# Kernel tuning notes

Measured on AMD Instinct MI355X. Metric: run time of the kernel, lower is better.

The kernel has to match this reference:

```python
import jax, jax.numpy as jnp
import numpy as np

B, N, C = 2, 8192, 768
H, K = 12, 256
D = C // H
HID = 4 * C
EPS = 1e-6

def layer_norm(x, w, b):
    mu = jnp.mean(x, axis=-1, keepdims=True)
    var = jnp.mean(jnp.square(x - mu), axis=-1, keepdims=True)
    return (x - mu) * jax.lax.rsqrt(var + EPS) * w + b

def setup_inputs() -> dict:
    key = jax.random.key(0)
    ks = jax.random.split(key, 8)
    s = 0.02
    return {
        "x": jax.random.normal(ks[0], (B, N, C), jnp.float32),
        "ln1_w": jnp.ones((C,), jnp.float32),
        "ln1_b": jnp.zeros((C,), jnp.float32),
        "qkv_w": jax.random.normal(ks[1], (C, 3 * C), jnp.float32) * s,
        "qkv_b": jnp.zeros((3 * C,), jnp.float32),
        "Ek": jax.random.normal(ks[2], (N, K), jnp.float32) * s,
        "Ev": jax.random.normal(ks[3], (N, K), jnp.float32) * s,
        "proj_w": jax.random.normal(ks[4], (C, C), jnp.float32) * s,
        "proj_b": jnp.zeros((C,), jnp.float32),
        "ln2_w": jnp.ones((C,), jnp.float32),
        "ln2_b": jnp.zeros((C,), jnp.float32),
        "fc1_w": jax.random.normal(ks[5], (C, HID), jnp.float32) * s,
        "fc1_b": jnp.zeros((HID,), jnp.float32),
        "fc2_w": jax.random.normal(ks[6], (HID, C), jnp.float32) * s,
        "fc2_b": jnp.zeros((C,), jnp.float32),
    }

def reference(x, ln1_w, ln1_b, qkv_w, qkv_b, Ek, Ev, proj_w, proj_b,
              ln2_w, ln2_b, fc1_w, fc1_b, fc2_w, fc2_b):
    scale = D ** -0.5
    # --- attention branch ---
    h = layer_norm(x, ln1_w, ln1_b)
    qkv = h @ qkv_w + qkv_b                      # (B,N,3C)
    qkv = qkv.reshape(B, N, 3, H, D).transpose(2, 0, 3, 1, 4)  # (3,B,H,N,D)
    q, k, v = qkv[0], qkv[1], qkv[2]
    # Linformer: project K/V along sequence dim N -> K
    k_proj = jnp.einsum('bhnd,nk->bhkd', k, Ek)
    v_proj = jnp.einsum('bhnd,nk->bhkd', v, Ev)
    logits = jnp.einsum('bhnd,bhkd->bhnk', q, k_proj) * scale
    logits = jnp.clip(logits, -50.0, 50.0)
    attn = jax.nn.softmax(logits, axis=-1)
    o = jnp.einsum('bhnk,bhkd->bhnd', attn, v_proj)
    o = o.transpose(0, 2, 1, 3).reshape(B, N, C)
    o = o @ proj_w + proj_b
    x = x + o                                    # alpha_attn = 1.0
    # --- MLP branch ---
    h = layer_norm(x, ln2_w, ln2_b)
    h = jax.nn.gelu(h @ fc1_w + fc1_b, approximate=False)
    h = h @ fc2_w + fc2_b
    return x + h                                 # alpha_mlp = 1.0
```

## Files before the change

### kernel.cpp

```cpp
#include <hip/hip_runtime.h>
#include <cstdint>

#define DEV __device__ __forceinline__

typedef __bf16 bf16x8 __attribute__((ext_vector_type(8)));
typedef float f32x4 __attribute__((ext_vector_type(4)));

DEV uint16_t f2bf(float f) {
  uint32_t u = __float_as_uint(f);
  u += 0x7FFFu + ((u >> 16) & 1u);
  return (uint16_t)(u >> 16);
}
DEV float bf2f(uint16_t h) { return __uint_as_float(((uint32_t)h) << 16); }

DEV void gload16(const void* g, void* l) {
  __builtin_amdgcn_global_load_lds((const __attribute__((address_space(1))) void*)g,
                                   (__attribute__((address_space(3))) void*)l, 16, 0, 0);
}

template <int N> DEV void waitcnt_vm() {
  if constexpr (N == 0) asm volatile("s_waitcnt vmcnt(0)" ::: "memory");
  else if constexpr (N == 4) asm volatile("s_waitcnt vmcnt(4)" ::: "memory");
  else if constexpr (N == 6) asm volatile("s_waitcnt vmcnt(6)" ::: "memory");
  else static_assert(N == 0 || N == 4 || N == 6, "unsupported vmcnt");
}

DEV float gelu_f(float v) {
  float u = v * (0.7978845608f + 0.0356774081f * v * v);
  return v / (1.f + __expf(-2.f * u));
}

__global__ __launch_bounds__(256) void ln768(const float* __restrict__ x,
                                             const float* __restrict__ w,
                                             const float* __restrict__ b,
                                             uint16_t* __restrict__ out) {
  const size_t row = blockIdx.x;
  const float* xr = x + row * 768;
  const int t = threadIdx.x;
  float v0 = xr[t], v1 = xr[t + 256], v2 = xr[t + 512];
  float s = v0 + v1 + v2;
  float s2 = v0 * v0 + v1 * v1 + v2 * v2;
#pragma unroll
  for (int o = 32; o; o >>= 1) {
    s += __shfl_down(s, o);
    s2 += __shfl_down(s2, o);
  }
  __shared__ float sh[8];
  if ((t & 63) == 0) { sh[t >> 6] = s; sh[4 + (t >> 6)] = s2; }
  __syncthreads();
  s = sh[0] + sh[1] + sh[2] + sh[3];
  s2 = sh[4] + sh[5] + sh[6] + sh[7];
  const float mu = s * (1.f / 768.f);
  const float var = s2 * (1.f / 768.f) - mu * mu;
  const float rstd = rsqrtf(var + 1e-6f);
  uint16_t* orow = out + row * 768;
  orow[t]       = f2bf((v0 - mu) * rstd * w[t] + b[t]);
  orow[t + 256] = f2bf((v1 - mu) * rstd * w[t + 256] + b[t + 256]);
  orow[t + 512] = f2bf((v2 - mu) * rstd * w[t + 512] + b[t + 512]);
}

__global__ __launch_bounds__(256) void transpose_f2b(const float* __restrict__ in,
                                                     uint16_t* __restrict__ outp,
                                                     int ldin, int ldout) {
  __shared__ float tile[32][33];
  const int tx = threadIdx.x, ty = threadIdx.y;
  const size_t x = (size_t)blockIdx.x * 32 + tx;
  const size_t y = (size_t)blockIdx.y * 32 + ty;
#pragma unroll
  for (int j = 0; j < 4; ++j) tile[ty + j * 8][tx] = in[(y + j * 8) * ldin + x];
  __syncthreads();
  const size_t x2 = (size_t)blockIdx.y * 32 + tx;
  const size_t y2 = (size_t)blockIdx.x * 32 + ty;
#pragma unroll
  for (int j = 0; j < 4; ++j) outp[(y2 + j * 8) * ldout + x2] = f2bf(tile[tx][ty + j * 8]);
}

__global__ __launch_bounds__(256) void transpose_b2b(const uint16_t* __restrict__ in,
                                                     uint16_t* __restrict__ outp,
                                                     int ldin, int ldout) {
  __shared__ uint16_t tile[32][33];
  const int tx = threadIdx.x, ty = threadIdx.y;
  const size_t x = (size_t)blockIdx.x * 32 + tx;
  const size_t y = (size_t)blockIdx.y * 32 + ty;
#pragma unroll
  for (int j = 0; j < 4; ++j) tile[ty + j * 8][tx] = in[(y + j * 8) * ldin + x];
  __syncthreads();
  const size_t x2 = (size_t)blockIdx.y * 32 + tx;
  const size_t y2 = (size_t)blockIdx.x * 32 + ty;
#pragma unroll
  for (int j = 0; j < 4; ++j) outp[(y2 + j * 8) * ldout + x2] = tile[tx][ty + j * 8];
}

__global__ __launch_bounds__(256) void kv_tn(const uint16_t* __restrict__ EkT,
                                             const uint16_t* __restrict__ EvT,
                                             const uint16_t* __restrict__ qkv,
                                             float* __restrict__ part) {
  const int bid = blockIdx.x;
  const int wg = (bid & 7) * 96 + (bid >> 3);
  const int inner = wg & 15;
  const int kt = inner & 3, ns = inner >> 2;
  const int rest = wg >> 4;
  const int ct = rest % 12, kvb = rest / 12;
  const int kv = kvb >> 1, b = kvb & 1;
  const int k0 = kt * 64, c0 = ct * 64, nsb = ns * 2048;

  const uint16_t* E = kv ? EvT : EkT;
  const uint16_t* KV = qkv + (size_t)b * 8192 * 2304 + 768 + kv * 768 + c0;
  const int tid = threadIdx.x, wave = tid >> 6, lane = tid & 63;
  const int l16 = lane & 15, lhi = lane >> 4;
  const int wm = wave >> 1, wn = wave & 1;

  f32x4 acc[2][2];
#pragma unroll
  for (int m = 0; m < 2; ++m)
#pragma unroll
    for (int n = 0; n < 2; ++n) acc[m][n] = f32x4{0.f, 0.f, 0.f, 0.f};

  const uint16_t* Eb = E + (size_t)(k0 + wm * 32 + l16) * 8192 + nsb + lhi * 8;
  const uint16_t* KVb = KV + ((size_t)nsb + lhi * 8) * 2304 + wn * 32 + l16;

  for (int n0 = 0; n0 < 2048; n0 += 32) {
    bf16x8 ef[2];
    ef[0] = *(const bf16x8*)(Eb + n0);
    ef[1] = *(const bf16x8*)(Eb + 16 * 8192 + n0);
    bf16x8 vf[2];
#pragma unroll
    for (int nf = 0; nf < 2; ++nf) {
      const uint16_t* p = KVb + (size_t)n0 * 2304 + nf * 16;
      union { bf16x8 v; uint16_t u[8]; } tu;
#pragma unroll
      for (int j = 0; j < 8; ++j) tu.u[j] = p[(size_t)j * 2304];
      vf[nf] = tu.v;
    }
#pragma unroll
    for (int m = 0; m < 2; ++m)
#pragma unroll
      for (int nf = 0; nf < 2; ++nf)
        acc[m][nf] = __builtin_amdgcn_mfma_f32_16x16x32_bf16(ef[m], vf[nf], acc[m][nf], 0, 0, 0);
  }

  float* outp = part + ((size_t)ns * 4 + kvb) * 196608;
#pragma unroll
  for (int m = 0; m < 2; ++m)
#pragma unroll
    for (int nf = 0; nf < 2; ++nf)
#pragma unroll
      for (int r = 0; r < 4; ++r)
        outp[(size_t)(k0 + wm * 32 + m * 16 + lhi * 4 + r) * 768 + c0 + wn * 32 + nf * 16 + l16] =
            acc[m][nf][r];
}

__global__ __launch_bounds__(256) void kv_reduce(const float* __restrict__ part,
                                                 uint16_t* __restrict__ kproj) {
  const int kvb = blockIdx.y;
  const int i = blockIdx.x * 256 + threadIdx.x;
  const float* p = part + (size_t)kvb * 196608 + i;
  float s = p[0] + p[786432] + p[2 * 786432] + p[3 * 786432];
  kproj[(size_t)kvb * 196608 + i] = f2bf(s);
}

__global__ __launch_bounds__(256, 3) void attn_fused(
    const uint16_t* __restrict__ qkv,
    const uint16_t* __restrict__ kproj,
    const uint16_t* __restrict__ vprojT,
    uint16_t* __restrict__ o) {
  const int bh = blockIdx.y;
  const int b = bh / 12, h = bh % 12;
  const int n0 = blockIdx.x * 64;
  const int tid = threadIdx.x, wave = tid >> 6, lane = tid & 63;
  const int l16 = lane & 15, lhi = lane >> 4;
  const int wm = wave >> 1, wn = wave & 1;

  __shared__ __align__(16) uint16_t sP[64 * 256];
  __shared__ float redm[2][64], reds[2][64], recs[64];

  const uint16_t* Kp = kproj + (size_t)b * 196608 + h * 64;
  const uint16_t* Qp = qkv + ((size_t)b * 8192 + n0) * 2304 + h * 64;
  const uint16_t* Vp = vprojT + ((size_t)b * 768 + h * 64) * 256;

  f32x4 st[8][2];
#pragma unroll
  for (int m = 0; m < 8; ++m)
#pragma unroll
    for (int nf = 0; nf < 2; ++nf) st[m][nf] = f32x4{0.f, 0.f, 0.f, 0.f};
#pragma unroll
  for (int ks = 0; ks < 2; ++ks) {
    bf16x8 kf[8], qf[2];
#pragma unroll
    for (int m = 0; m < 8; ++m) {
      const int kvi = wm * 128 + m * 16 + l16;
      kf[m] = *(const bf16x8*)(Kp + (size_t)kvi * 768 + ks * 32 + lhi * 8);
    }
#pragma unroll
    for (int nf = 0; nf < 2; ++nf) {
      const int n = wn * 32 + nf * 16 + l16;
      qf[nf] = *(const bf16x8*)(Qp + (size_t)n * 2304 + ks * 32 + lhi * 8);
    }
#pragma unroll
    for (int m = 0; m < 8; ++m)
#pragma unroll
      for (int nf = 0; nf < 2; ++nf)
        st[m][nf] = __builtin_amdgcn_mfma_f32_16x16x32_bf16(kf[m], qf[nf], st[m][nf], 0, 0, 0);
  }

  float pmax[2] = {-50.f, -50.f};
#pragma unroll
  for (int m = 0; m < 8; ++m)
#pragma unroll
    for (int nf = 0; nf < 2; ++nf)
#pragma unroll
      for (int r = 0; r < 4; ++r) {
        float v = fminf(fmaxf(st[m][nf][r] * 0.125f, -50.f), 50.f);
        st[m][nf][r] = v;
        pmax[nf] = fmaxf(pmax[nf], v);
      }
#pragma unroll
  for (int nf = 0; nf < 2; ++nf) {
    pmax[nf] = fmaxf(pmax[nf], __shfl_xor(pmax[nf], 16));
    pmax[nf] = fmaxf(pmax[nf], __shfl_xor(pmax[nf], 32));
  }
  if (lhi == 0) {
#pragma unroll
    for (int nf = 0; nf < 2; ++nf) redm[wm][wn * 32 + nf * 16 + l16] = pmax[nf];
  }
  __syncthreads();
  float M[2];
#pragma unroll
  for (int nf = 0; nf < 2; ++nf) {
    const int col = wn * 32 + nf * 16 + l16;
    M[nf] = fmaxf(redm[0][col], redm[1][col]);
  }

  float psum[2] = {0.f, 0.f};
#pragma unroll
  for (int m = 0; m < 8; ++m) {
#pragma unroll
    for (int nf = 0; nf < 2; ++nf) {
      float e0 = __expf(st[m][nf][0] - M[nf]);
      float e1 = __expf(st[m][nf][1] - M[nf]);
      float e2 = __expf(st[m][nf][2] - M[nf]);
      float e3 = __expf(st[m][nf][3] - M[nf]);
      psum[nf] += (e0 + e1) + (e2 + e3);
      uint2 pk;
      pk.x = (uint32_t)f2bf(e0) | ((uint32_t)f2bf(e1) << 16);
      pk.y = (uint32_t)f2bf(e2) | ((uint32_t)f2bf(e3) << 16);
      const int n = wn * 32 + nf * 16 + l16;
      const int kvb2 = (wm * 128 + m * 16 + lhi * 4) * 2;
      *(uint2*)((char*)sP + n * 512 + (kvb2 ^ ((n & 7) << 4))) = pk;
    }
  }
#pragma unroll
  for (int nf = 0; nf < 2; ++nf) {
    psum[nf] += __shfl_xor(psum[nf], 16);
    psum[nf] += __shfl_xor(psum[nf], 32);
  }
  if (lhi == 0) {
#pragma unroll
    for (int nf = 0; nf < 2; ++nf) reds[wm][wn * 32 + nf * 16 + l16] = psum[nf];
  }
  __syncthreads();
  if (wm == 0 && lhi == 0) {
#pragma unroll
    for (int nf = 0; nf < 2; ++nf) {
      const int col = wn * 32 + nf * 16 + l16;
      recs[col] = 1.f / (reds[0][col] + reds[1][col]);
    }
  }
  __syncthreads();

  f32x4 pacc[2][2];
#pragma unroll
  for (int mf = 0; mf < 2; ++mf)
#pragma unroll
    for (int nf = 0; nf < 2; ++nf) pacc[mf][nf] = f32x4{0.f, 0.f, 0.f, 0.f};
#pragma unroll
  for (int ks = 0; ks < 8; ++ks) {
    bf16x8 pa[2], vb[2];
#pragma unroll
    for (int mf = 0; mf < 2; ++mf) {
      const int n = wm * 32 + mf * 16 + l16;
      pa[mf] = *(const bf16x8*)((char*)sP + n * 512 + ((ks * 64 + lhi * 16) ^ ((n & 7) << 4)));
    }
#pragma unroll
    for (int nf = 0; nf < 2; ++nf) {
      const int d = wn * 32 + nf * 16 + l16;
      vb[nf] = *(const bf16x8*)(Vp + (size_t)d * 256 + ks * 32 + lhi * 8);
    }
#pragma unroll
    for (int mf = 0; mf < 2; ++mf)
#pragma unroll
      for (int nf = 0; nf < 2; ++nf)
        pacc[mf][nf] = __builtin_amdgcn_mfma_f32_16x16x32_bf16(pa[mf], vb[nf], pacc[mf][nf], 0, 0, 0);
  }
  uint16_t* orow = o + ((size_t)b * 8192 + n0) * 768 + h * 64;
#pragma unroll
  for (int mf = 0; mf < 2; ++mf) {
#pragma unroll
    for (int r = 0; r < 4; ++r) {
      const int n = wm * 32 + mf * 16 + lhi * 4 + r;
      const float inv = recs[n];
#pragma unroll
      for (int nf = 0; nf < 2; ++nf) {
        const int d = wn * 32 + nf * 16 + l16;
        orow[(size_t)n * 768 + d] = f2bf(pacc[mf][nf][r] * inv);
      }
    }
  }
}

template <int BM, int BN, bool OUTBF, bool HASBIAS, bool DOGELU, bool HASRES>
__global__ __launch_bounds__(512, 2) void gemm3(
    const uint16_t* __restrict__ A, const uint16_t* __restrict__ B,
    void* __restrict__ Cbase, const float* __restrict__ bias,
    const float* __restrict__ res, int Kd, int lda, int ldb, int ldc) {
  constexpr int WROWS = BM / 4, WCOLS = BN / 2;
  constexpr int FM = WROWS / 16, FN = WCOLS / 16;
  constexpr int IA = BM / 64, IB = BN / 64;
  constexpr int LPT = IA + IB;
  constexpr int ABUF = BM * 64, BBUF = BN * 64;
  __shared__ __align__(16) uint16_t lds[3 * (ABUF + BBUF)];

  const int nn = gridDim.y;
  const int nwg = gridDim.x * gridDim.y;
  const int bid = blockIdx.y * gridDim.x + blockIdx.x;
  const int q = nwg >> 3, r8 = nwg & 7, xcd = bid & 7, idx = bid >> 3;
  const int wg = (xcd < r8 ? xcd * (q + 1) : r8 * (q + 1) + (xcd - r8) * q) + idx;
  const int bm = wg / nn, bn = wg % nn;
  const int row0 = bm * BM, col0 = bn * BN;

  const int tid = threadIdx.x;
  const int wave = tid >> 6, lane = tid & 63;
  const int wm = wave >> 1, wn = wave & 1;
  const int l16 = lane & 15, lhi = lane >> 4;
  const int srow = tid >> 3, sslot = tid & 7;

  auto stageA = [&](uint16_t* sa, int k0, int j) {
    const int rw = j * 64 + srow;
    const int sp = sslot ^ (rw & 7);
    gload16(A + (size_t)(row0 + rw) * lda + k0 + sp * 8, sa + rw * 64 + sslot * 8);
  };
  auto stageB = [&](uint16_t* sb, int k0, int j) {
    const int rw = j * 64 + srow;
    const int sp = sslot ^ (rw & 7);
    gload16(B + (size_t)(col0 + rw) * ldb + k0 + sp * 8, sb + rw * 64 + sslot * 8);
  };

  f32x4 acc[FM][FN];
#pragma unroll
  for (int m = 0; m < FM; ++m)
#pragma unroll
    for (int n = 0; n < FN; ++n) acc[m][n] = f32x4{0.f, 0.f, 0.f, 0.f};

  const int NT = Kd >> 6;
#pragma unroll
  for (int j = 0; j < IA; ++j) stageA(lds, 0, j);
#pragma unroll
  for (int j = 0; j < IB; ++j) stageB(lds + ABUF, 0, j);
#pragma unroll
  for (int j = 0; j < IA; ++j) stageA(lds + (ABUF + BBUF), 64, j);
#pragma unroll
  for (int j = 0; j < IB; ++j) stageB(lds + (ABUF + BBUF) + ABUF, 64, j);

  for (int t = 0; t < NT; ++t) {
    if (t < NT - 1) waitcnt_vm<LPT>();
    else waitcnt_vm<0>();
    __builtin_amdgcn_s_barrier();
    asm volatile("" ::: "memory");
    const uint16_t* sa = lds + (t % 3) * (ABUF + BBUF);
    const uint16_t* sb = sa + ABUF;
    uint16_t* pa = lds + ((t + 2) % 3) * (ABUF + BBUF);
    uint16_t* pb = pa + ABUF;
    const bool pf = (t + 2) < NT;
    const int k0p = (t + 2) * 64;

    if (pf) {
#pragma unroll
      for (int j = 0; j < IA / 2; ++j) stageA(pa, k0p, j);
#pragma unroll
      for (int j = 0; j < IB / 2; ++j) stageB(pb, k0p, j);
    }
    {
      bf16x8 af[FM], bfr[FN];
#pragma unroll
      for (int n = 0; n < FN; ++n) {
        const int rw = wn * WCOLS + n * 16 + l16;
        bfr[n] = *(const bf16x8*)(sb + rw * 64 + ((lhi) ^ (rw & 7)) * 8);
      }
#pragma unroll
      for (int m = 0; m < FM; ++m) {
        const int rw = wm * WROWS + m * 16 + l16;
        af[m] = *(const bf16x8*)(sa + rw * 64 + ((lhi) ^ (rw & 7)) * 8);
      }
      __builtin_amdgcn_s_setprio(1);
#pragma unroll
      for (int m = 0; m < FM; ++m)
#pragma unroll
        for (int n = 0; n < FN; ++n)
          acc[m][n] = __builtin_amdgcn_mfma_f32_16x16x32_bf16(af[m], bfr[n], acc[m][n], 0, 0, 0);
      __builtin_amdgcn_s_setprio(0);
    }
    if (pf) {
#pragma unroll
      for (int j = IA / 2; j < IA; ++j) stageA(pa, k0p, j);
#pragma unroll
      for (int j = IB / 2; j < IB; ++j) stageB(pb, k0p, j);
    }
    {
      bf16x8 af[FM], bfr[FN];
#pragma unroll
      for (int n = 0; n < FN; ++n) {
        const int rw = wn * WCOLS + n * 16 + l16;
        bfr[n] = *(const bf16x8*)(sb + rw * 64 + ((4 + lhi) ^ (rw & 7)) * 8);
      }
#pragma unroll
      for (int m = 0; m < FM; ++m) {
        const int rw = wm * WROWS + m * 16 + l16;
        af[m] = *(const bf16x8*)(sa + rw * 64 + ((4 + lhi) ^ (rw & 7)) * 8);
      }
      __builtin_amdgcn_s_setprio(1);
#pragma unroll
      for (int m = 0; m < FM; ++m)
#pragma unroll
        for (int n = 0; n < FN; ++n)
          acc[m][n] = __builtin_amdgcn_mfma_f32_16x16x32_bf16(af[m], bfr[n], acc[m][n], 0, 0, 0);
      __builtin_amdgcn_s_setprio(0);
    }
  }

  float* Cf = (float*)Cbase;
  uint16_t* Cb = (uint16_t*)Cbase;
#pragma unroll
  for (int m = 0; m < FM; ++m) {
#pragma unroll
    for (int n = 0; n < FN; ++n) {
      const int col = col0 + wn * WCOLS + n * 16 + l16;
      float bv = 0.f;
      if (HASBIAS) bv = bias[col];
#pragma unroll
      for (int r = 0; r < 4; ++r) {
        const int row = row0 + wm * WROWS + m * 16 + lhi * 4 + r;
        float v = acc[m][n][r] + bv;
        if (DOGELU) v = gelu_f(v);
        const size_t cidx = (size_t)row * ldc + col;
        if (HASRES) v += res[cidx];
        if (OUTBF) Cb[cidx] = f2bf(v);
        else Cf[cidx] = v;
      }
    }
  }
}

extern "C" void kernel_launch(void* const* d_in, const int* in_sizes, int n_in,
                              void* d_out, int out_size, void* d_ws, size_t ws_size,
                              hipStream_t stream) {
  const float* x      = (const float*)d_in[0];
  const float* ln1_w  = (const float*)d_in[1];
  const float* ln1_b  = (const float*)d_in[2];
  const float* qkv_w  = (const float*)d_in[3];
  const float* qkv_b  = (const float*)d_in[4];
  const float* Ek     = (const float*)d_in[5];
  const float* Ev     = (const float*)d_in[6];
  const float* proj_w = (const float*)d_in[7];
  const float* proj_b = (const float*)d_in[8];
  const float* ln2_w  = (const float*)d_in[9];
  const float* ln2_b  = (const float*)d_in[10];
  const float* fc1_w  = (const float*)d_in[11];
  const float* fc1_b  = (const float*)d_in[12];
  const float* fc2_w  = (const float*)d_in[13];
  const float* fc2_b  = (const float*)d_in[14];
  float* out = (float*)d_out;

  char* w8 = (char*)d_ws;
  size_t off = 0;
  auto take = [&](size_t bytes) { char* p = w8 + off; off += bytes; return p; };
  uint16_t* qkv_wT  = (uint16_t*)take(2304ull * 768 * 2);
  uint16_t* proj_wT = (uint16_t*)take(768ull * 768 * 2);
  uint16_t* fc1_wT  = (uint16_t*)take(3072ull * 768 * 2);
  uint16_t* fc2_wT  = (uint16_t*)take(768ull * 3072 * 2);
  uint16_t* EkT     = (uint16_t*)take(256ull * 8192 * 2);
  uint16_t* EvT     = (uint16_t*)take(256ull * 8192 * 2);
  uint16_t* h_bf    = (uint16_t*)take(16384ull * 768 * 2);
  uint16_t* qkv_bf  = (uint16_t*)take(16384ull * 2304 * 2);
  uint16_t* big     = (uint16_t*)take(100663296ull);
  uint16_t* kproj   = (uint16_t*)take(2ull * 2 * 256 * 768 * 2);
  uint16_t* vprojT  = (uint16_t*)take(2ull * 768 * 256 * 2);
  uint16_t* o_bf    = (uint16_t*)take(16384ull * 768 * 2);
  float* part = (float*)big;
  (void)ws_size; (void)in_sizes; (void)n_in; (void)out_size;

  const dim3 tb(32, 8);
  transpose_f2b<<<dim3(72, 24), tb, 0, stream>>>(qkv_w, qkv_wT, 2304, 768);
  transpose_f2b<<<dim3(24, 24), tb, 0, stream>>>(proj_w, proj_wT, 768, 768);
  transpose_f2b<<<dim3(96, 24), tb, 0, stream>>>(fc1_w, fc1_wT, 3072, 768);
  transpose_f2b<<<dim3(24, 96), tb, 0, stream>>>(fc2_w, fc2_wT, 768, 3072);
  transpose_f2b<<<dim3(8, 256), tb, 0, stream>>>(Ek, EkT, 256, 8192);
  transpose_f2b<<<dim3(8, 256), tb, 0, stream>>>(Ev, EvT, 256, 8192);
  ln768<<<16384, 256, 0, stream>>>(x, ln1_w, ln1_b, h_bf);
  gemm3<256, 128, true, true, false, false><<<dim3(64, 18), 512, 0, stream>>>(
      h_bf, qkv_wT, qkv_bf, qkv_b, nullptr, 768, 768, 768, 2304);
  kv_tn<<<768, 256, 0, stream>>>(EkT, EvT, qkv_bf, part);
  kv_reduce<<<dim3(768, 4), 256, 0, stream>>>(part, kproj);
  for (int b = 0; b < 2; ++b)
    transpose_b2b<<<dim3(24, 8), tb, 0, stream>>>(
        kproj + (size_t)(2 + b) * 196608, vprojT + (size_t)b * 768 * 256, 768, 256);
  attn_fused<<<dim3(128, 24), 256, 0, stream>>>(qkv_bf, kproj, vprojT, o_bf);
  gemm3<128, 128, false, true, false, true><<<dim3(128, 6), 512, 0, stream>>>(
      o_bf, proj_wT, out, proj_b, x, 768, 768, 768, 768);
  ln768<<<16384, 256, 0, stream>>>(out, ln2_w, ln2_b, h_bf);
  gemm3<256, 128, true, true, true, false><<<dim3(64, 24), 512, 0, stream>>>(
      h_bf, fc1_wT, big, fc1_b, nullptr, 768, 768, 768, 3072);
  gemm3<128, 128, false, true, false, true><<<dim3(128, 6), 512, 0, stream>>>(
      big, fc2_wT, out, fc2_b, out, 3072, 3072, 3072, 768);
}
```

Measured before the change: 489.9 us.

## Replace GEMM kernels with 256x256-tile double-buffered GEMM using split-K half planes

The templated triple-buffered GEMM is replaced by a fixed 256x256 tile kernel with an 8-wave 2x4 layout. Each 64-wide K tile is staged as two 32-wide half planes into a double buffer with a new swizzle, and loads of the next tile are interleaved with the MFMA sub-steps under more barriers. Larger tiles raise arithmetic intensity and cut global traffic per FLOP. In exchange the grids shrink a lot (e.g. 192 blocks for the proj/fc2 GEMMs on a 256-CU part), which risks underfilling the GPU, and the 128-accumulator register footprint is higher.

```diff
diff --git a/kernel.cpp b/kernel.cpp
--- a/kernel.cpp
+++ b/kernel.cpp
@@ -21,8 +21,7 @@
 template <int N> DEV void waitcnt_vm() {
   if constexpr (N == 0) asm volatile("s_waitcnt vmcnt(0)" ::: "memory");
   else if constexpr (N == 4) asm volatile("s_waitcnt vmcnt(4)" ::: "memory");
-  else if constexpr (N == 6) asm volatile("s_waitcnt vmcnt(6)" ::: "memory");
-  else static_assert(N == 0 || N == 4 || N == 6, "unsupported vmcnt");
+  else static_assert(N == 0 || N == 4, "unsupported vmcnt");
 }
 
 DEV float gelu_f(float v) {
@@ -160,10 +159,8 @@
 }
 
 __global__ __launch_bounds__(256, 3) void attn_fused(
-    const uint16_t* __restrict__ qkv,
-    const uint16_t* __restrict__ kproj,
-    const uint16_t* __restrict__ vprojT,
-    uint16_t* __restrict__ o) {
+    const uint16_t* __restrict__ qkv, const uint16_t* __restrict__ kproj,
+    const uint16_t* __restrict__ vprojT, uint16_t* __restrict__ o) {
   const int bh = blockIdx.y;
   const int b = bh / 12, h = bh % 12;
   const int n0 = blockIdx.x * 64;
@@ -308,17 +305,14 @@
   }
 }
 
-template <int BM, int BN, bool OUTBF, bool HASBIAS, bool DOGELU, bool HASRES>
-__global__ __launch_bounds__(512, 2) void gemm3(
+template <bool OUTBF, bool HASBIAS, bool DOGELU, bool HASRES>
+__global__ __launch_bounds__(512, 2) void gemm256(
     const uint16_t* __restrict__ A, const uint16_t* __restrict__ B,
     void* __restrict__ Cbase, const float* __restrict__ bias,
     const float* __restrict__ res, int Kd, int lda, int ldb, int ldc) {
-  constexpr int WROWS = BM / 4, WCOLS = BN / 2;
-  constexpr int FM = WROWS / 16, FN = WCOLS / 16;
-  constexpr int IA = BM / 64, IB = BN / 64;
-  constexpr int LPT = IA + IB;
-  constexpr int ABUF = BM * 64, BBUF = BN * 64;
-  __shared__ __align__(16) uint16_t lds[3 * (ABUF + BBUF)];
+  constexpr int PLANE = 8192;
+  constexpr int BUF = 4 * PLANE;
+  __shared__ __align__(16) uint16_t lds[2 * BUF];
 
   const int nn = gridDim.y;
   const int nwg = gridDim.x * gridDim.y;
@@ -326,119 +320,98 @@
   const int q = nwg >> 3, r8 = nwg & 7, xcd = bid & 7, idx = bid >> 3;
   const int wg = (xcd < r8 ? xcd * (q + 1) : r8 * (q + 1) + (xcd - r8) * q) + idx;
   const int bm = wg / nn, bn = wg % nn;
-  const int row0 = bm * BM, col0 = bn * BN;
+  const int row0 = bm * 256, col0 = bn * 256;
 
   const int tid = threadIdx.x;
   const int wave = tid >> 6, lane = tid & 63;
-  const int wm = wave >> 1, wn = wave & 1;
+  const int wm = wave >> 2, wn = wave & 3;
   const int l16 = lane & 15, lhi = lane >> 4;
-  const int srow = tid >> 3, sslot = tid & 7;
-
-  auto stageA = [&](uint16_t* sa, int k0, int j) {
-    const int rw = j * 64 + srow;
-    const int sp = sslot ^ (rw & 7);
-    gload16(A + (size_t)(row0 + rw) * lda + k0 + sp * 8, sa + rw * 64 + sslot * 8);
+  const int srow = tid >> 2, sq = tid & 3;
+
+  auto stage = [&](int b, int t, int op, int kh) {
+    const int k0 = t * 64 + kh * 32;
+    const uint16_t* G = op ? B : A;
+    const int ld = op ? ldb : lda;
+    const int r0 = op ? col0 : row0;
+    uint16_t* dst = lds + b * BUF + op * 2 * PLANE + kh * PLANE;
+#pragma unroll
+    for (int j = 0; j < 2; ++j) {
+      const int rw = j * 128 + srow;
+      const int sl = sq ^ ((rw >> 1) & 3);
+      gload16(G + (size_t)(r0 + rw) * ld + k0 + sl * 8, dst + rw * 32 + sq * 8);
+    }
   };
-  auto stageB = [&](uint16_t* sb, int k0, int j) {
-    const int rw = j * 64 + srow;
-    const int sp = sslot ^ (rw & 7);
-    gload16(B + (size_t)(col0 + rw) * ldb + k0 + sp * 8, sb + rw * 64 + sslot * 8);
+  auto rdA = [&](const uint16_t* buf, int ks, int mh, int m) -> bf16x8 {
+    const int rw = wm * 128 + mh * 64 + m * 16 + l16;
+    const int sl = lhi ^ ((rw >> 1) & 3);
+    return *(const bf16x8*)(buf + ks * PLANE + rw * 32 + sl * 8);
   };
-
-  f32x4 acc[FM][FN];
-#pragma unroll
-  for (int m = 0; m < FM; ++m)
-#pragma unroll
-    for (int n = 0; n < FN; ++n) acc[m][n] = f32x4{0.f, 0.f, 0.f, 0.f};
+  auto rdB = [&](const uint16_t* buf, int ks, int n) -> bf16x8 {
+    const int rw = wn * 64 + n * 16 + l16;
+    const int sl = lhi ^ ((rw >> 1) & 3);
+    return *(const bf16x8*)(buf + 2 * PLANE + ks * PLANE + rw * 32 + sl * 8);
+  };
+
+  f32x4 acc[8][4];
+#pragma unroll
+  for (int m = 0; m < 8; ++m)
+#pragma unroll
+    for (int n = 0; n < 4; ++n) acc[m][n] = f32x4{0.f, 0.f, 0.f, 0.f};
 
   const int NT = Kd >> 6;
-#pragma unroll
-  for (int j = 0; j < IA; ++j) stageA(lds, 0, j);
-#pragma unroll
-  for (int j = 0; j < IB; ++j) stageB(lds + ABUF, 0, j);
-#pragma unroll
-  for (int j = 0; j < IA; ++j) stageA(lds + (ABUF + BBUF), 64, j);
-#pragma unroll
-  for (int j = 0; j < IB; ++j) stageB(lds + (ABUF + BBUF) + ABUF, 64, j);
-
-  for (int t = 0; t < NT; ++t) {
-    if (t < NT - 1) waitcnt_vm<LPT>();
-    else waitcnt_vm<0>();
-    __builtin_amdgcn_s_barrier();
-    asm volatile("" ::: "memory");
-    const uint16_t* sa = lds + (t % 3) * (ABUF + BBUF);
-    const uint16_t* sb = sa + ABUF;
-    uint16_t* pa = lds + ((t + 2) % 3) * (ABUF + BBUF);
-    uint16_t* pb = pa + ABUF;
-    const bool pf = (t + 2) < NT;
-    const int k0p = (t + 2) * 64;
-
-    if (pf) {
-#pragma unroll
-      for (int j = 0; j < IA / 2; ++j) stageA(pa, k0p, j);
-#pragma unroll
-      for (int j = 0; j < IB / 2; ++j) stageB(pb, k0p, j);
-    }
-    {
-      bf16x8 af[FM], bfr[FN];
-#pragma unroll
-      for (int n = 0; n < FN; ++n) {
-        const int rw = wn * WCOLS + n * 16 + l16;
-        bfr[n] = *(const bf16x8*)(sb + rw * 64 + ((lhi) ^ (rw & 7)) * 8);
+  stage(0, 0, 0, 0); stage(0, 0, 1, 0); stage(0, 0, 0, 1); stage(0, 0, 1, 1);
+  waitcnt_vm<4>();
+  __builtin_amdgcn_s_barrier();
+  asm volatile("" ::: "memory");
+
+  for (int u = 0; u < NT; ++u) {
+    const uint16_t* cb = lds + (u & 1) * BUF;
+    const int nb = (u + 1) & 1;
+    const bool st = (u + 1) < NT;
+    bf16x8 bfr[4], afr[4];
+#pragma unroll
+    for (int ks = 0; ks < 2; ++ks) {
+#pragma unroll
+      for (int mh = 0; mh < 2; ++mh) {
+        if (mh == 0) {
+#pragma unroll
+          for (int n = 0; n < 4; ++n) bfr[n] = rdB(cb, ks, n);
+        }
+#pragma unroll
+        for (int m = 0; m < 4; ++m) afr[m] = rdA(cb, ks, mh, m);
+        if (st) stage(nb, u + 1, mh, ks);
+        __builtin_amdgcn_s_barrier();
+        asm volatile("" ::: "memory");
+        __builtin_amdgcn_s_setprio(1);
+#pragma unroll
+        for (int m = 0; m < 4; ++m)
+#pragma unroll
+          for (int n = 0; n < 4; ++n)
+            acc[mh * 4 + m][n] =
+                __builtin_amdgcn_mfma_f32_16x16x32_bf16(afr[m], bfr[n], acc[mh * 4 + m][n], 0, 0, 0);
+        __builtin_amdgcn_s_setprio(0);
+        if (mh == 1) {
+          if (st) waitcnt_vm<4>();
+          else waitcnt_vm<0>();
+        }
+        __builtin_amdgcn_s_barrier();
+        asm volatile("" ::: "memory");
       }
-#pragma unroll
-      for (int m = 0; m < FM; ++m) {
-        const int rw = wm * WROWS + m * 16 + l16;
-        af[m] = *(const bf16x8*)(sa + rw * 64 + ((lhi) ^ (rw & 7)) * 8);
-      }
-      __builtin_amdgcn_s_setprio(1);
-#pragma unroll
-      for (int m = 0; m < FM; ++m)
-#pragma unroll
-        for (int n = 0; n < FN; ++n)
-          acc[m][n] = __builtin_amdgcn_mfma_f32_16x16x32_bf16(af[m], bfr[n], acc[m][n], 0, 0, 0);
-      __builtin_amdgcn_s_setprio(0);
-    }
-    if (pf) {
-#pragma unroll
-      for (int j = IA / 2; j < IA; ++j) stageA(pa, k0p, j);
-#pragma unroll
-      for (int j = IB / 2; j < IB; ++j) stageB(pb, k0p, j);
-    }
-    {
-      bf16x8 af[FM], bfr[FN];
-#pragma unroll
-      for (int n = 0; n < FN; ++n) {
-        const int rw = wn * WCOLS + n * 16 + l16;
-        bfr[n] = *(const bf16x8*)(sb + rw * 64 + ((4 + lhi) ^ (rw & 7)) * 8);
-      }
-#pragma unroll
-      for (int m = 0; m < FM; ++m) {
-        const int rw = wm * WROWS + m * 16 + l16;
-        af[m] = *(const bf16x8*)(sa + rw * 64 + ((4 + lhi) ^ (rw & 7)) * 8);
-      }
-      __builtin_amdgcn_s_setprio(1);
-#pragma unroll
-      for (int m = 0; m < FM; ++m)
-#pragma unroll
-        for (int n = 0; n < FN; ++n)
-          acc[m][n] = __builtin_amdgcn_mfma_f32_16x16x32_bf16(af[m], bfr[n], acc[m][n], 0, 0, 0);
-      __builtin_amdgcn_s_setprio(0);
     }
   }
 
   float* Cf = (float*)Cbase;
   uint16_t* Cb = (uint16_t*)Cbase;
 #pragma unroll
-  for (int m = 0; m < FM; ++m) {
-#pragma unroll
-    for (int n = 0; n < FN; ++n) {
-      const int col = col0 + wn * WCOLS + n * 16 + l16;
+  for (int m = 0; m < 8; ++m) {
+#pragma unroll
+    for (int n = 0; n < 4; ++n) {
+      const int col = col0 + wn * 64 + n * 16 + l16;
       float bv = 0.f;
       if (HASBIAS) bv = bias[col];
 #pragma unroll
       for (int r = 0; r < 4; ++r) {
-        const int row = row0 + wm * WROWS + m * 16 + lhi * 4 + r;
+        const int row = row0 + wm * 128 + m * 16 + lhi * 4 + r;
         float v = acc[m][n][r] + bv;
         if (DOGELU) v = gelu_f(v);
         const size_t cidx = (size_t)row * ldc + col;
@@ -496,7 +469,7 @@
   transpose_f2b<<<dim3(8, 256), tb, 0, stream>>>(Ek, EkT, 256, 8192);
   transpose_f2b<<<dim3(8, 256), tb, 0, stream>>>(Ev, EvT, 256, 8192);
   ln768<<<16384, 256, 0, stream>>>(x, ln1_w, ln1_b, h_bf);
-  gemm3<256, 128, true, true, false, false><<<dim3(64, 18), 512, 0, stream>>>(
+  gemm256<true, true, false, false><<<dim3(64, 9), 512, 0, stream>>>(
       h_bf, qkv_wT, qkv_bf, qkv_b, nullptr, 768, 768, 768, 2304);
   kv_tn<<<768, 256, 0, stream>>>(EkT, EvT, qkv_bf, part);
   kv_reduce<<<dim3(768, 4), 256, 0, stream>>>(part, kproj);
@@ -504,11 +477,11 @@
     transpose_b2b<<<dim3(24, 8), tb, 0, stream>>>(
         kproj + (size_t)(2 + b) * 196608, vprojT + (size_t)b * 768 * 256, 768, 256);
   attn_fused<<<dim3(128, 24), 256, 0, stream>>>(qkv_bf, kproj, vprojT, o_bf);
-  gemm3<128, 128, false, true, false, true><<<dim3(128, 6), 512, 0, stream>>>(
+  gemm256<false, true, false, true><<<dim3(64, 3), 512, 0, stream>>>(
       o_bf, proj_wT, out, proj_b, x, 768, 768, 768, 768);
   ln768<<<16384, 256, 0, stream>>>(out, ln2_w, ln2_b, h_bf);
-  gemm3<256, 128, true, true, true, false><<<dim3(64, 24), 512, 0, stream>>>(
+  gemm256<true, true, true, false><<<dim3(64, 12), 512, 0, stream>>>(
       h_bf, fc1_wT, big, fc1_b, nullptr, 768, 768, 768, 3072);
-  gemm3<128, 128, false, true, false, true><<<dim3(128, 6), 512, 0, stream>>>(
+  gemm256<false, true, false, true><<<dim3(64, 3), 512, 0, stream>>>(
       big, fc2_wT, out, fc2_b, out, 3072, 3072, 3072, 768);
 }
```

Result: slower. 524.5 us (+7.1%).
